# Performance work log

Hardware: AMD Instinct MI355X
Metric: run time of the kernel (lower is better)

Reference implementation:

```python
import jax, jax.numpy as jnp
import numpy as np

B, S, H, I, G = 2, 1024, 1024, 4096, 8


def setup_inputs() -> dict:
    key = jax.random.key(0)
    k1, k2, k3, k4 = jax.random.split(key, 4)
    # kaiming-style scaled init (scale matters only for numerics, not math)
    hidden_states = jax.random.normal(k1, (B, S, H), dtype=jnp.float32)
    WG = jax.random.normal(k2, (H, G), dtype=jnp.float32) * (1.0 / np.sqrt(H))
    Wi = jax.random.normal(k3, (G, H, I), dtype=jnp.float32) * (1.0 / np.sqrt(H))
    down = jax.random.normal(k4, (I, H), dtype=jnp.float32) * (1.0 / np.sqrt(I))
    return {"hidden_states": hidden_states, "WG": WG, "Wi": Wi, "down": down, "topk": 2}


def topk_sigmoid(gate, k):
    # gate: [B,S,G] -> sigmoid gated scores masked to top-k per token
    _, idx = jax.lax.top_k(gate, k)                       # idx: [B,S,k]
    mask = (idx[..., None] == jnp.arange(gate.shape[-1])).any(axis=-2)  # [B,S,G] bool
    return jax.nn.sigmoid(gate) * mask


def reference(hidden_states, WG, Wi, down, topk):
    gate = hidden_states @ WG                             # [B,S,G]
    g = topk_sigmoid(gate, topk)                          # [B,S,G]
    # dense contraction over all groups (faithful to original einsum)
    up = jnp.einsum('bse,bsg,geo->bso', hidden_states, g, Wi)  # [B,S,I]
    act = jnp.square(jax.nn.relu(up))                     # ReLU^2
    return act @ down                                     # [B,S,H]
```

## Files before the change

### kernel.cpp

```cpp
#include <hip/hip_runtime.h>
#include <hip/hip_bf16.h>

typedef unsigned short u16;
typedef short short8_t __attribute__((ext_vector_type(8)));
typedef float f32x4 __attribute__((ext_vector_type(4)));

#define GLOBAL_AS(p) ((const __attribute__((address_space(1))) void*)(p))
#define LDS_AS(p)    ((__attribute__((address_space(3))) void*)(p))

__device__ __forceinline__ u16 f2bf(float f) {
    union { float f; unsigned int u; } x;
    x.f = f;
    unsigned int r = x.u + 0x7fffu + ((x.u >> 16) & 1u);
    return (u16)(r >> 16);
}

#define M_NMT   0
#define M_TE    2
#define M_TB    42
#define M_PAIR  96
#define M_RTOK  4192
#define M_RW    9312

__global__ __launch_bounds__(64) void gate_topk_kernel(
    const float* __restrict__ h, const float* __restrict__ wg, float* __restrict__ w) {
    const int t = blockIdx.x;
    const int lane = threadIdx.x;
    float acc[8];
#pragma unroll
    for (int g = 0; g < 8; ++g) acc[g] = 0.f;
    for (int e = lane; e < 1024; e += 64) {
        float hv = h[(size_t)t * 1024 + e];
        float4 r0 = *(const float4*)&wg[e * 8];
        float4 r1 = *(const float4*)&wg[e * 8 + 4];
        acc[0] += hv * r0.x; acc[1] += hv * r0.y; acc[2] += hv * r0.z; acc[3] += hv * r0.w;
        acc[4] += hv * r1.x; acc[5] += hv * r1.y; acc[6] += hv * r1.z; acc[7] += hv * r1.w;
    }
#pragma unroll
    for (int off = 32; off > 0; off >>= 1) {
#pragma unroll
        for (int g = 0; g < 8; ++g) acc[g] += __shfl_down(acc[g], off);
    }
    if (lane == 0) {
        int i1 = 0;
        for (int g = 1; g < 8; ++g) if (acc[g] > acc[i1]) i1 = g;
        int i2 = -1;
        for (int g = 0; g < 8; ++g) {
            if (g == i1) continue;
            if (i2 < 0 || acc[g] > acc[i2]) i2 = g;
        }
#pragma unroll
        for (int g = 0; g < 8; ++g) {
            float v = (g == i1 || g == i2) ? (1.f / (1.f + __expf(-acc[g]))) : 0.f;
            w[t * 8 + g] = v;
        }
    }
}

__global__ __launch_bounds__(256) void scan_kernel(
    const float* __restrict__ w, int* __restrict__ meta) {
    __shared__ int cnt[8], pos[8];
    const int tid = threadIdx.x;
    if (tid < 8) cnt[tid] = 0;
    __syncthreads();
    for (int t = tid; t < 2048; t += 256) {
#pragma unroll
        for (int g = 0; g < 8; ++g)
            if (w[t * 8 + g] > 0.f) atomicAdd(&cnt[g], 1);
    }
    __syncthreads();
    if (tid == 0) {
        int base = 0, mt = 0;
        for (int e = 0; e < 8; ++e) {
            pos[e] = base;
            int nt = (cnt[e] + 127) >> 7;
            for (int k = 0; k < nt; ++k) { meta[M_TE + mt] = e; meta[M_TB + mt] = base + k * 128; ++mt; }
            base += nt << 7;
        }
        meta[M_NMT] = mt;
        meta[1] = base;
    }
    __syncthreads();
    for (int i = tid; i < 5120; i += 256) meta[M_RTOK + i] = -1;
    __syncthreads();
    float* row_w = (float*)&meta[M_RW];
    for (int t = tid; t < 2048; t += 256) {
        int slot = 0;
#pragma unroll
        for (int g = 0; g < 8; ++g) {
            float wv = w[t * 8 + g];
            if (wv > 0.f) {
                int p = atomicAdd(&pos[g], 1);
                meta[M_RTOK + p] = t;
                row_w[p] = wv;
                meta[M_PAIR + t * 2 + slot] = p;
                ++slot;
            }
        }
    }
}

__global__ __launch_bounds__(256) void gather_a_kernel(
    const float* __restrict__ h, const int* __restrict__ meta, u16* __restrict__ A) {
    const int row = blockIdx.x;
    const int tid = threadIdx.x;
    const int tok = meta[M_RTOK + row];
    u16* dst = A + (size_t)row * 1024;
    if (tok < 0) {
        uint2 z; z.x = 0u; z.y = 0u;
        ((uint2*)dst)[tid] = z;
        return;
    }
    const float wv = ((const float*)&meta[M_RW])[row];
    float4 v = ((const float4*)(h + (size_t)tok * 1024))[tid];
    u16 o[4] = { f2bf(v.x * wv), f2bf(v.y * wv), f2bf(v.z * wv), f2bf(v.w * wv) };
    ((uint2*)dst)[tid] = *(const uint2*)o;
}

__global__ __launch_bounds__(256) void gemm1_sparse_kernel(
    const u16* __restrict__ A, const float* __restrict__ Wi,
    float* __restrict__ up, const int* __restrict__ meta) {
    const int mt = blockIdx.y;
    if (mt >= meta[M_NMT]) return;
    const int e = meta[M_TE + mt];
    const int base = meta[M_TB + mt];
    const int n0 = blockIdx.x * 128;
    const int K = 1024, N = 4096;
    const float* Bm = Wi + (size_t)e * K * N;

    __shared__ short a_tile[128 * 64];
    __shared__ short b_tile[128 * 64];
    const int tid = threadIdx.x;
    const int lane = tid & 63;
    const int wave = tid >> 6;
    const int wm = (wave >> 1) * 64;
    const int wn = (wave & 1) * 64;
    const int r = lane & 15;
    const int quad = lane >> 4;
    const int rowin = lane >> 3;
    const int achk = ((lane & 7) ^ (rowin & 7)) * 8;
    const int aldst = (lane & 7) * 8;

    const int bidx_n = tid & 127;
    const int bidx_k8 = tid >> 7;

    const f32x4 vzero = {0.f, 0.f, 0.f, 0.f};
    f32x4 acc[4][4];
#pragma unroll
    for (int i = 0; i < 4; ++i)
#pragma unroll
        for (int j = 0; j < 4; ++j) acc[i][j] = vzero;

    float bv[4][8];
#pragma unroll
    for (int cb = 0; cb < 4; ++cb) {
        const float* bp = Bm + (size_t)((bidx_k8 + cb * 2) * 8) * N + n0 + bidx_n;
#pragma unroll
        for (int kk = 0; kk < 8; ++kk) bv[cb][kk] = bp[(size_t)kk * N];
    }

    for (int kb = 0; kb < K; kb += 64) {
#pragma unroll
        for (int it = 0; it < 4; ++it) {
            int row = wave * 8 + it * 32 + rowin;
            const u16* ga = A + (size_t)(base + row) * K + kb + achk;
            __builtin_amdgcn_global_load_lds(GLOBAL_AS(ga), LDS_AS(&a_tile[row * 64 + aldst]), 16, 0, 0);
        }
#pragma unroll
        for (int cb = 0; cb < 4; ++cb) {
            int bk8 = bidx_k8 + cb * 2;
            u16 bc[8];
#pragma unroll
            for (int kk = 0; kk < 8; ++kk) bc[kk] = f2bf(bv[cb][kk]);
            *(short8_t*)&b_tile[bidx_n * 64 + ((bk8 ^ (bidx_n & 7)) * 8)] = *(const short8_t*)bc;
        }
        __syncthreads();

        if (kb + 64 < K) {
#pragma unroll
            for (int cb = 0; cb < 4; ++cb) {
                const float* bp = Bm + (size_t)(kb + 64 + (bidx_k8 + cb * 2) * 8) * N + n0 + bidx_n;
#pragma unroll
                for (int kk = 0; kk < 8; ++kk) bv[cb][kk] = bp[(size_t)kk * N];
            }
        }

#pragma unroll
        for (int ks = 0; ks < 2; ++ks) {
            const int cp = ((ks * 4 + quad) ^ (r & 7)) * 8;
            short8_t af[4], bfr[4];
#pragma unroll
            for (int i = 0; i < 4; ++i)
                af[i] = *(const short8_t*)&a_tile[(wm + i * 16 + r) * 64 + cp];
#pragma unroll
            for (int j = 0; j < 4; ++j)
                bfr[j] = *(const short8_t*)&b_tile[(wn + j * 16 + r) * 64 + cp];
#pragma unroll
            for (int i = 0; i < 4; ++i)
#pragma unroll
                for (int j = 0; j < 4; ++j)
                    acc[i][j] = __builtin_amdgcn_mfma_f32_16x16x32_bf16(af[i], bfr[j], acc[i][j], 0, 0, 0);
        }
        __syncthreads();
    }
#pragma unroll
    for (int i = 0; i < 4; ++i)
#pragma unroll
        for (int j = 0; j < 4; ++j)
#pragma unroll
            for (int reg = 0; reg < 4; ++reg) {
                int cr = base + wm + i * 16 + quad * 4 + reg;
                int cc = n0 + wn + j * 16 + r;
                up[(size_t)cr * N + cc] = acc[i][j][reg];
            }
}

__global__ __launch_bounds__(256) void combine_kernel(
    const float* __restrict__ up, const int* __restrict__ meta, u16* __restrict__ act) {
    const int t = blockIdx.x;
    const int tid = threadIdx.x;
    const int p0 = meta[M_PAIR + t * 2];
    const int p1 = meta[M_PAIR + t * 2 + 1];
    const float* r0 = up + (size_t)p0 * 4096;
    const float* r1 = up + (size_t)p1 * 4096;
    u16* dst = act + (size_t)t * 4096;
#pragma unroll
    for (int it = 0; it < 4; ++it) {
        int i = (tid + it * 256) * 4;
        float4 a = *(const float4*)&r0[i];
        float4 b = *(const float4*)&r1[i];
        float s0 = a.x + b.x, s1 = a.y + b.y, s2 = a.z + b.z, s3 = a.w + b.w;
        s0 = s0 > 0.f ? s0 * s0 : 0.f;
        s1 = s1 > 0.f ? s1 * s1 : 0.f;
        s2 = s2 > 0.f ? s2 * s2 : 0.f;
        s3 = s3 > 0.f ? s3 * s3 : 0.f;
        u16 o[4] = { f2bf(s0), f2bf(s1), f2bf(s2), f2bf(s3) };
        *(uint2*)&dst[i] = *(const uint2*)o;
    }
}

__global__ __launch_bounds__(256) void transpose_cvt_kernel(
    const float* __restrict__ in, u16* __restrict__ out, int R, int C) {
    __shared__ u16 tile[64][65];
    const int rt = blockIdx.y * 64;
    const int ct = blockIdx.x * 64;
    const int tid = threadIdx.x;
#pragma unroll
    for (int it = 0; it < 2; ++it) {
        int r = (tid >> 3) + it * 32;
        int c8 = (tid & 7) * 8;
        const float* ip = &in[(size_t)(rt + r) * C + ct + c8];
        float4 v0 = *(const float4*)ip;
        float4 v1 = *(const float4*)(ip + 4);
        tile[c8 + 0][r] = f2bf(v0.x); tile[c8 + 1][r] = f2bf(v0.y);
        tile[c8 + 2][r] = f2bf(v0.z); tile[c8 + 3][r] = f2bf(v0.w);
        tile[c8 + 4][r] = f2bf(v1.x); tile[c8 + 5][r] = f2bf(v1.y);
        tile[c8 + 6][r] = f2bf(v1.z); tile[c8 + 7][r] = f2bf(v1.w);
    }
    __syncthreads();
#pragma unroll
    for (int it = 0; it < 2; ++it) {
        int c = (tid >> 3) + it * 32;
        int r8 = (tid & 7) * 8;
        u16 tmp[8];
#pragma unroll
        for (int j = 0; j < 8; ++j) tmp[j] = tile[c][r8 + j];
        *(uint4*)&out[(size_t)(ct + c) * R + rt + r8] = *(const uint4*)tmp;
    }
}

template <int BM, int WROWS, int WCOLS>
__global__ __launch_bounds__(256) void gemm_tn_kernel(
    const u16* __restrict__ X, const u16* __restrict__ Y, float* __restrict__ Cout,
    int M, int N, int K) {
    constexpr int WM = BM / WROWS;
    constexpr int WN = 128 / WCOLS;
    constexpr int FI = WM / 16;
    constexpr int FJ = WN / 16;
    __shared__ short a_tile[2][BM * 64];
    __shared__ short b_tile[2][128 * 64];
    const int tid = threadIdx.x;
    const int lane = tid & 63;
    const int wave = tid >> 6;

    const int Nt = gridDim.x, Mt = gridDim.y;
    const int lid = blockIdx.y * Nt + blockIdx.x;
    const int xcd = lid & 7;
    const int p = lid >> 3;
    const int n_tile = xcd * (Nt >> 3) + p / Mt;
    const int m_tile = p % Mt;
    const int m0 = m_tile * BM;
    const int n0 = n_tile * 128;

    const int wm = (wave / WCOLS) * WM;
    const int wn = (wave % WCOLS) * WN;
    const int rowin = lane >> 3;
    const int achk = ((lane & 7) ^ (rowin & 7)) * 8;
    const int aldst = (lane & 7) * 8;
    const int r = lane & 15;
    const int quad = lane >> 4;

    const f32x4 vzero = {0.f, 0.f, 0.f, 0.f};
    f32x4 acc[FI][FJ];
#pragma unroll
    for (int i = 0; i < FI; ++i)
#pragma unroll
        for (int j = 0; j < FJ; ++j) acc[i][j] = vzero;

#define G2_STAGE(kb_, buf)                                                            \
    {                                                                                 \
        const int kbc = (kb_);                                                        \
        _Pragma("unroll")                                                             \
        for (int it = 0; it < BM / 32; ++it) {                                        \
            int row = wave * 8 + it * 32 + rowin;                                     \
            const u16* ga = X + (size_t)(m0 + row) * K + kbc + achk;                  \
            __builtin_amdgcn_global_load_lds(GLOBAL_AS(ga),                           \
                LDS_AS(&a_tile[buf][row * 64 + aldst]), 16, 0, 0);                    \
        }                                                                             \
        _Pragma("unroll")                                                             \
        for (int it = 0; it < 4; ++it) {                                              \
            int row = wave * 8 + it * 32 + rowin;                                     \
            const u16* gb = Y + (size_t)(n0 + row) * K + kbc + achk;                  \
            __builtin_amdgcn_global_load_lds(GLOBAL_AS(gb),                           \
                LDS_AS(&b_tile[buf][row * 64 + aldst]), 16, 0, 0);                    \
        }                                                                             \
    }

#define G2_COMPUTE(buf)                                                               \
    {                                                                                 \
        _Pragma("unroll")                                                             \
        for (int ks = 0; ks < 2; ++ks) {                                              \
            const int cp = ((ks * 4 + quad) ^ (r & 7)) * 8;                           \
            short8_t af[FI], bfr[FJ];                                                 \
            _Pragma("unroll")                                                         \
            for (int i = 0; i < FI; ++i)                                              \
                af[i] = *(const short8_t*)&a_tile[buf][(wm + i * 16 + r) * 64 + cp];  \
            _Pragma("unroll")                                                         \
            for (int j = 0; j < FJ; ++j)                                              \
                bfr[j] = *(const short8_t*)&b_tile[buf][(wn + j * 16 + r) * 64 + cp]; \
            _Pragma("unroll")                                                         \
            for (int i = 0; i < FI; ++i)                                              \
                _Pragma("unroll")                                                     \
                for (int j = 0; j < FJ; ++j)                                          \
                    acc[i][j] = __builtin_amdgcn_mfma_f32_16x16x32_bf16(              \
                        af[i], bfr[j], acc[i][j], 0, 0, 0);                           \
        }                                                                             \
    }

    const int nk = K >> 6;
    G2_STAGE(0, 0);
    __syncthreads();
    for (int t = 0; t < nk - 1; ++t) {
        const int nxt = (t + 1) & 1;
        G2_STAGE((t + 1) * 64, nxt);
        G2_COMPUTE(t & 1);
        __syncthreads();
    }
    G2_COMPUTE((nk - 1) & 1);

#undef G2_STAGE
#undef G2_COMPUTE

#pragma unroll
    for (int i = 0; i < FI; ++i)
#pragma unroll
        for (int j = 0; j < FJ; ++j)
#pragma unroll
            for (int reg = 0; reg < 4; ++reg) {
                int cr = m0 + wm + i * 16 + quad * 4 + reg;
                int cc = n0 + wn + j * 16 + r;
                Cout[(size_t)cr * N + cc] = acc[i][j][reg];
            }
}

extern "C" void kernel_launch(void* const* d_in, const int* in_sizes, int n_in,
                              void* d_out, int out_size, void* d_ws, size_t ws_size,
                              hipStream_t stream) {
    const float* h    = (const float*)d_in[0];
    const float* WG   = (const float*)d_in[1];
    const float* Wi   = (const float*)d_in[2];
    const float* down = (const float*)d_in[3];
    float* out = (float*)d_out;

    const int T = 2048, H = 1024, I = 4096;

    char* ws = (char*)d_ws;
    float* w_gate = (float*)(ws);
    int*   meta   = (int*)(ws + 65536);
    u16*   Arow   = (u16*)(ws + 131072);
    float* up     = (float*)(ws + 131072 + 10485760);
    u16*   act    = (u16*)(ws + 131072 + 10485760 + 83886080);
    u16*   downT  = (u16*)(ws + 131072 + 10485760 + 83886080 + 16777216);

    gate_topk_kernel<<<T, 64, 0, stream>>>(h, WG, w_gate);
    scan_kernel<<<1, 256, 0, stream>>>(w_gate, meta);
    gather_a_kernel<<<5120, 256, 0, stream>>>(h, meta, Arow);

    gemm1_sparse_kernel<<<dim3(32, 40), 256, 0, stream>>>(Arow, Wi, up, meta);

    combine_kernel<<<T, 256, 0, stream>>>(up, meta, act);

    transpose_cvt_kernel<<<dim3(H / 64, I / 64), 256, 0, stream>>>(down, downT, I, H);
    gemm_tn_kernel<32, 1, 4><<<dim3(H / 128, T / 32), 256, 0, stream>>>(
        act, downT, out, T, H, I);
}
```

Before: 357.7 us.

## Split-K the down-projection GEMM with larger tiles and add a reduction kernel

After: 344.0 us. -3.8%, faster.

```diff
diff --git a/kernel.cpp b/kernel.cpp
--- a/kernel.cpp
+++ b/kernel.cpp
@@ -57,13 +57,13 @@
     }
 }
 
-__global__ __launch_bounds__(256) void scan_kernel(
+__global__ __launch_bounds__(1024) void scan_kernel(
     const float* __restrict__ w, int* __restrict__ meta) {
     __shared__ int cnt[8], pos[8];
     const int tid = threadIdx.x;
     if (tid < 8) cnt[tid] = 0;
     __syncthreads();
-    for (int t = tid; t < 2048; t += 256) {
+    for (int t = tid; t < 2048; t += 1024) {
 #pragma unroll
         for (int g = 0; g < 8; ++g)
             if (w[t * 8 + g] > 0.f) atomicAdd(&cnt[g], 1);
@@ -81,10 +81,10 @@
         meta[1] = base;
     }
     __syncthreads();
-    for (int i = tid; i < 5120; i += 256) meta[M_RTOK + i] = -1;
+    for (int i = tid; i < 5120; i += 1024) meta[M_RTOK + i] = -1;
     __syncthreads();
     float* row_w = (float*)&meta[M_RW];
-    for (int t = tid; t < 2048; t += 256) {
+    for (int t = tid; t < 2048; t += 1024) {
         int slot = 0;
 #pragma unroll
         for (int g = 0; g < 8; ++g) {
@@ -271,7 +271,7 @@
 
 template <int BM, int WROWS, int WCOLS>
 __global__ __launch_bounds__(256) void gemm_tn_kernel(
-    const u16* __restrict__ X, const u16* __restrict__ Y, float* __restrict__ Cout,
+    const u16* __restrict__ X, const u16* __restrict__ Y, float* __restrict__ Pout,
     int M, int N, int K) {
     constexpr int WM = BM / WROWS;
     constexpr int WN = 128 / WCOLS;
@@ -291,6 +291,8 @@
     const int m_tile = p % Mt;
     const int m0 = m_tile * BM;
     const int n0 = n_tile * 128;
+    const int kchunk = K >> 2;
+    const int kb0 = blockIdx.z * kchunk;
 
     const int wm = (wave / WCOLS) * WM;
     const int wn = (wave % WCOLS) * WN;
@@ -347,12 +349,12 @@
         }                                                                             \
     }
 
-    const int nk = K >> 6;
-    G2_STAGE(0, 0);
+    const int nk = kchunk >> 6;
+    G2_STAGE(kb0, 0);
     __syncthreads();
     for (int t = 0; t < nk - 1; ++t) {
         const int nxt = (t + 1) & 1;
-        G2_STAGE((t + 1) * 64, nxt);
+        G2_STAGE(kb0 + (t + 1) * 64, nxt);
         G2_COMPUTE(t & 1);
         __syncthreads();
     }
@@ -361,6 +363,7 @@
 #undef G2_STAGE
 #undef G2_COMPUTE
 
+    float* Co = Pout + (size_t)blockIdx.z * M * N;
 #pragma unroll
     for (int i = 0; i < FI; ++i)
 #pragma unroll
@@ -369,8 +372,24 @@
             for (int reg = 0; reg < 4; ++reg) {
                 int cr = m0 + wm + i * 16 + quad * 4 + reg;
                 int cc = n0 + wn + j * 16 + r;
-                Cout[(size_t)cr * N + cc] = acc[i][j][reg];
+                Co[(size_t)cr * N + cc] = acc[i][j][reg];
             }
+}
+
+__global__ __launch_bounds__(256) void reduce4_kernel(
+    const float* __restrict__ P, float* __restrict__ out) {
+    const size_t S = (size_t)2048 * 1024;
+    size_t i = ((size_t)blockIdx.x * 256 + threadIdx.x) * 4;
+    float4 a = *(const float4*)&P[i];
+    float4 b = *(const float4*)&P[S + i];
+    float4 c = *(const float4*)&P[2 * S + i];
+    float4 d = *(const float4*)&P[3 * S + i];
+    float4 o;
+    o.x = (a.x + b.x) + (c.x + d.x);
+    o.y = (a.y + b.y) + (c.y + d.y);
+    o.z = (a.z + b.z) + (c.z + d.z);
+    o.w = (a.w + b.w) + (c.w + d.w);
+    *(float4*)&out[i] = o;
 }
 
 extern "C" void kernel_launch(void* const* d_in, const int* in_sizes, int n_in,
@@ -391,9 +410,10 @@
     float* up     = (float*)(ws + 131072 + 10485760);
     u16*   act    = (u16*)(ws + 131072 + 10485760 + 83886080);
     u16*   downT  = (u16*)(ws + 131072 + 10485760 + 83886080 + 16777216);
+    float* part   = up;
 
     gate_topk_kernel<<<T, 64, 0, stream>>>(h, WG, w_gate);
-    scan_kernel<<<1, 256, 0, stream>>>(w_gate, meta);
+    scan_kernel<<<1, 1024, 0, stream>>>(w_gate, meta);
     gather_a_kernel<<<5120, 256, 0, stream>>>(h, meta, Arow);
 
     gemm1_sparse_kernel<<<dim3(32, 40), 256, 0, stream>>>(Arow, Wi, up, meta);
@@ -401,6 +421,7 @@
     combine_kernel<<<T, 256, 0, stream>>>(up, meta, act);
 
     transpose_cvt_kernel<<<dim3(H / 64, I / 64), 256, 0, stream>>>(down, downT, I, H);
-    gemm_tn_kernel<32, 1, 4><<<dim3(H / 128, T / 32), 256, 0, stream>>>(
-        act, downT, out, T, H, I);
-}
+    gemm_tn_kernel<128, 2, 2><<<dim3(H / 128, T / 128, 4), 256, 0, stream>>>(
+        act, downT, part, T, H, I);
+    reduce4_kernel<<<(T * H) / 1024, 256, 0, stream>>>(part, out);
+}
```
